# Performance work log

Measured on AMD Instinct MI355X. Metric: run time of the kernel, lower is better.

The kernel has to match this reference:

```python
import jax, jax.numpy as jnp
import numpy as np

NUM_QUBITS = 16
N_LAYERS = 3
N_PARAMS = 6
BATCH = 64
DIM = 2 ** NUM_QUBITS


def setup_inputs() -> dict:
    key = jax.random.key(0)
    k1, k2, k3, k4, k5 = jax.random.split(key, 5)
    sr = jax.random.normal(k1, (BATCH, DIM), jnp.float32)
    si = jax.random.normal(k2, (BATCH, DIM), jnp.float32)
    nrm = jnp.sqrt(jnp.sum(sr * sr + si * si, axis=1, keepdims=True))
    sr, si = sr / nrm, si / nrm  # StatePrep requires normalized states
    var_params = jax.random.normal(k3, (N_LAYERS, NUM_QUBITS, N_PARAMS), jnp.float32)
    head_w = jax.random.normal(k4, (1, NUM_QUBITS), jnp.float32) / np.sqrt(NUM_QUBITS)
    head_b = jax.random.normal(k5, (1,), jnp.float32) * 0.01
    return {"state_real": sr, "state_imag": si, "var_params": var_params,
            "head_w": head_w, "head_b": head_b}


def _rot_unitary(tx, ty, tz):
    # Fused single-qubit unitary U = RZ(tz) @ RY(ty) @ RX(tx)
    cx, sx = jnp.cos(tx / 2), jnp.sin(tx / 2)
    cy, sy = jnp.cos(ty / 2), jnp.sin(ty / 2)
    Rx = jnp.stack([jnp.stack([cx + 0j, -1j * sx]),
                    jnp.stack([-1j * sx, cx + 0j])])
    Ry = jnp.stack([jnp.stack([cy + 0j, -sy + 0j]),
                    jnp.stack([sy + 0j, cy + 0j])])
    ez = jnp.exp(-1j * tz / 2)
    zero = jnp.zeros_like(ez)
    Rz = jnp.stack([jnp.stack([ez, zero]), jnp.stack([zero, jnp.conj(ez)])])
    return (Rz @ Ry @ Rx).astype(jnp.complex64)


def _circuit_features(state_real, state_imag, var_params):
    psi = jax.lax.complex(state_real, state_imag)  # (B, 2^n), wire 0 = MSB
    B = psi.shape[0]
    for l in range(N_LAYERS):
        for q in range(NUM_QUBITS):
            U = _rot_unitary(var_params[l, q, 0], var_params[l, q, 1], var_params[l, q, 2])
            psi = psi.reshape(B, 2 ** q, 2, -1)  # isolate wire q
            psi = jnp.einsum('ij,bljr->blir', U, psi)
        for q in range(NUM_QUBITS - 1):
            # CNOT(control=q, target=q+1): flip target axis where control=1
            psi = psi.reshape(B, 2 ** q, 2, 2, -1)
            psi = jnp.concatenate([psi[:, :, 0:1], psi[:, :, 1:2, ::-1]], axis=2)
        psi = psi.reshape(B, -1)
    probs = psi.real ** 2 + psi.imag ** 2  # (B, 2^n)
    feats = []
    for q in range(NUM_QUBITS):
        p = probs.reshape(B, 2 ** q, 2, -1)
        feats.append(p[:, :, 0, :].sum(axis=(1, 2)) - p[:, :, 1, :].sum(axis=(1, 2)))
    return jnp.stack(feats, axis=1)  # (B, n) expvals of PauliZ


def reference(state_real, state_imag, var_params, head_w, head_b):
    feats = _circuit_features(state_real, state_imag, var_params)
    return (feats @ head_w.T + head_b)[:, 0]  # (B,)
```

## Files before the change

### kernel.cpp

```cpp
#include <hip/hip_runtime.h>


struct G8 { float r00,i00,r01,i01,r10,i10,r11,i11; };

__device__ __forceinline__ G8 loadG(const float* p) {
  G8 g;
  g.r00=p[0]; g.i00=p[1]; g.r01=p[2]; g.i01=p[3];
  g.r10=p[4]; g.i10=p[5]; g.r11=p[6]; g.i11=p[7];
  return g;
}

__device__ __forceinline__ void cmul2(const G8& g, float& r0, float& i0, float& r1, float& i1) {
  const float nr0 = g.r00*r0 - g.i00*i0 + g.r01*r1 - g.i01*i1;
  const float ni0 = g.r00*i0 + g.i00*r0 + g.r01*i1 + g.i01*r1;
  const float nr1 = g.r10*r0 - g.i10*i0 + g.r11*r1 - g.i11*i1;
  const float ni1 = g.r10*i0 + g.i10*r0 + g.r11*i1 + g.i11*r1;
  r0=nr0; i0=ni0; r1=nr1; i1=ni1;
}

__device__ __forceinline__ void cgate(const G8& g, int flip,
                                      float& r0, float& i0, float& r1, float& i1) {
  if (flip) cmul2(g, r1, i1, r0, i0);
  else      cmul2(g, r0, i0, r1, i1);
}

__device__ __forceinline__ void supd(const G8& g, int w, float& xr_, float& xi_,
                                     float pr, float pi_) {
  const float dr = w ? g.r11 : g.r00, di = w ? g.i11 : g.i00;
  const float br = w ? g.r10 : g.r01, bi = w ? g.i10 : g.i01;
  const float nr = dr*xr_ - di*xi_ + br*pr - bi*pi_;
  const float ni = dr*xi_ + di*xr_ + br*pi_ + bi*pr;
  xr_ = nr; xi_ = ni;
}

__device__ __forceinline__ void buildU(const float* __restrict__ vp, float* U) {
  const int i = threadIdx.x;
  if (i < 48) {
    const float tx = vp[i*6+0], ty = vp[i*6+1], tz = vp[i*6+2];
    float sx, cx, sy, cy, sz, cz;
    sincosf(0.5f*tx, &sx, &cx);
    sincosf(0.5f*ty, &sy, &cy);
    sincosf(0.5f*tz, &sz, &cz);
    const float m00r = cy*cx,  m00i = sy*sx;
    const float m01r = -sy*cx, m01i = -cy*sx;
    const float m10r = sy*cx,  m10i = -cy*sx;
    const float m11r = cy*cx,  m11i = -sy*sx;
    float* o = U + i*8;
    o[0] = cz*m00r + sz*m00i;  o[1] = cz*m00i - sz*m00r;
    o[2] = cz*m01r + sz*m01i;  o[3] = cz*m01i - sz*m01r;
    o[4] = cz*m10r - sz*m10i;  o[5] = cz*m10i + sz*m10r;
    o[6] = cz*m11r - sz*m11i;  o[7] = cz*m11i + sz*m11r;
  }
}

#define GU(l, w) loadG(Ush + ((l)*16 + (w))*8)

__global__ void __launch_bounds__(256, 2)
kA(const float* __restrict__ sr, const float* __restrict__ si,
   float* __restrict__ dr, float* __restrict__ di,
   const float* __restrict__ vp, const float* __restrict__ hb, float* __restrict__ out) {
  __shared__ float Ush[384];
  buildU(vp, Ush);
  const int t = threadIdx.x;
  const int l = t & 63, wv = t >> 6;
  const int l5 = (l >> 5) & 1, l4 = (l >> 4) & 1;
  const int b = blockIdx.x >> 3, c = blockIdx.x & 7;
  if (blockIdx.x == 0 && t < 64) out[t] = hb[0];
  __syncthreads();

  const size_t bb = (size_t)b << 16;
  const int tb = (l5 << 10) | (l4 << 9) | (c << 6) | (wv << 4) | (l & 15);
  float xr[32], xi[32];
  #pragma unroll
  for (int k = 0; k < 32; ++k) {
    xr[k] = sr[bb + (k << 11) + tb];
    xi[k] = si[bb + (k << 11) + tb];
  }

  #pragma unroll
  for (int g = 0; g < 5; ++g) {
    const int kb = 4 - g;
    const G8 U = GU(0, g);
    #pragma unroll
    for (int p = 0; p < 16; ++p) {
      const int i0 = ((p >> kb) << (kb + 1)) | (p & ((1 << kb) - 1));
      cmul2(U, xr[i0], xi[i0], xr[i0 | (1 << kb)], xi[i0 | (1 << kb)]);
    }
  }
  { const G8 U = GU(0, 5);
    #pragma unroll
    for (int a = 0; a < 32; ++a) {
      const float pr = __shfl_xor(xr[a], 32), pi_ = __shfl_xor(xi[a], 32);
      supd(U, l5, xr[a], xi[a], pr, pi_);
    } }
  { const G8 U = GU(0, 6);
    #pragma unroll
    for (int a = 0; a < 32; ++a) {
      const float pr = __shfl_xor(xr[a], 16), pi_ = __shfl_xor(xi[a], 16);
      supd(U, l4, xr[a], xi[a], pr, pi_);
    } }
  { const G8 U = GU(1, 0);
    #pragma unroll
    for (int k = 0; k < 32; ++k) if (!((k >> 4) & 1))
      cmul2(U, xr[k], xi[k], xr[k^24], xi[k^24]); }
  { const G8 U = GU(1, 1);
    #pragma unroll
    for (int k = 0; k < 32; ++k) if (!((k >> 3) & 1))
      cgate(U, (k >> 4) & 1, xr[k], xi[k], xr[k^12], xi[k^12]); }
  { const G8 U = GU(1, 2);
    #pragma unroll
    for (int k = 0; k < 32; ++k) if (!((k >> 2) & 1))
      cgate(U, ((k>>4)^(k>>3)) & 1, xr[k], xi[k], xr[k^6], xi[k^6]); }
  { const G8 U = GU(1, 3);
    #pragma unroll
    for (int k = 0; k < 32; ++k) if (!((k >> 1) & 1))
      cgate(U, ((k>>4)^(k>>3)^(k>>2)) & 1, xr[k], xi[k], xr[k^3], xi[k^3]); }
  { const G8 U = GU(1, 4);
    #pragma unroll
    for (int m = 0; m < 16; ++m) {
      const int k0 = 2*m, k1 = 2*m + 1;
      const float p0r = __shfl_xor(xr[k1], 32), p0i = __shfl_xor(xi[k1], 32);
      const float p1r = __shfl_xor(xr[k0], 32), p1i = __shfl_xor(xi[k0], 32);
      const int w0 = __builtin_popcount(k0) & 1;
      supd(U, w0,     xr[k0], xi[k0], p0r, p0i);
      supd(U, w0 ^ 1, xr[k1], xi[k1], p1r, p1i);
    } }
  { const G8 U = GU(1, 5);
    #pragma unroll
    for (int k = 0; k < 32; ++k) {
      const float pr = __shfl_xor(xr[k], 48), pi_ = __shfl_xor(xi[k], 48);
      supd(U, (__builtin_popcount(k) ^ l5) & 1, xr[k], xi[k], pr, pi_);
    } }
  { const G8 U = GU(2, 0);
    #pragma unroll
    for (int k = 0; k < 32; ++k) if (!((k >> 4) & 1))
      cmul2(U, xr[k], xi[k], xr[k^20], xi[k^20]); }
  { const G8 U = GU(2, 1);
    #pragma unroll
    for (int k = 0; k < 32; ++k) if (!((k >> 3) & 1))
      cmul2(U, xr[k], xi[k], xr[k^10], xi[k^10]); }
  { const G8 U = GU(2, 2);
    #pragma unroll
    for (int k = 0; k < 32; ++k) if (!((k >> 2) & 1))
      cgate(U, (k >> 4) & 1, xr[k], xi[k], xr[k^5], xi[k^5]); }
  { const G8 U = GU(2, 3);
    #pragma unroll
    for (int k = 0; k < 32; ++k) if (!((k >> 1) & 1)) {
      const float p0r = __shfl_xor(xr[k^2], 32), p0i = __shfl_xor(xi[k^2], 32);
      const float p1r = __shfl_xor(xr[k],   32), p1i = __shfl_xor(xi[k],   32);
      const int w0 = (k >> 3) & 1;
      supd(U, w0,     xr[k],   xi[k],   p0r, p0i);
      supd(U, w0 ^ 1, xr[k^2], xi[k^2], p1r, p1i);
    } }

  #pragma unroll
  for (int k = 0; k < 32; ++k) {
    dr[bb + (k << 11) + tb] = xr[k];
    di[bb + (k << 11) + tb] = xi[k];
  }
}

__device__ __forceinline__ int SA(int a) { return a ^ ((a >> 6) & 3); }

__global__ void __launch_bounds__(256, 2)
kB(const float* __restrict__ sr, const float* __restrict__ si,
   const float* __restrict__ vp, const float* __restrict__ hw, float* __restrict__ out) {
  __shared__ float lds[8192];
  __shared__ float Ush[384];
  __shared__ float red[4];
  buildU(vp, Ush);
  const int t = threadIdx.x;
  const int l = t & 63, wv = t >> 6;
  const int b = blockIdx.x >> 4, h = blockIdx.x & 15;
  __syncthreads();

  const int ph = __builtin_popcount(h) & 1;
  const int pA = ((h >> 1) ^ (h >> 3)) & 1;
  const int pB = (h ^ (h >> 2)) & 1;
  const size_t base0 = ((size_t)b << 16) | (h << 12) | (wv << 8) | (l << 2);

  float xr[16], xi[16];
  #pragma unroll
  for (int k = 0; k < 4; ++k) {
    const float4 vr = *(const float4*)(sr + base0 + (k << 10));
    const float4 vi = *(const float4*)(si + base0 + (k << 10));
    xr[k*4+0]=vr.x; xr[k*4+1]=vr.y; xr[k*4+2]=vr.z; xr[k*4+3]=vr.w;
    xi[k*4+0]=vi.x; xi[k*4+1]=vi.y; xi[k*4+2]=vi.z; xi[k*4+3]=vi.w;
  }

  #pragma unroll
  for (int g = 0; g < 6; ++g) {
    const int mask = 32 >> g;
    const G8 U = GU(0, 8 + g);
    const int hi = (l >> (5 - g)) & 1;
    #pragma unroll
    for (int a = 0; a < 16; ++a) {
      const float pr = __shfl_xor(xr[a], mask), pi_ = __shfl_xor(xi[a], mask);
      supd(U, hi, xr[a], xi[a], pr, pi_);
    }
  }
  { const G8 U = GU(0, 14);
    #pragma unroll
    for (int k = 0; k < 4; ++k) {
      cmul2(U, xr[k*4+0], xi[k*4+0], xr[k*4+2], xi[k*4+2]);
      cmul2(U, xr[k*4+1], xi[k*4+1], xr[k*4+3], xi[k*4+3]);
    } }
  { const G8 U = GU(0, 15);
    #pragma unroll
    for (int k = 0; k < 4; ++k) {
      cmul2(U, xr[k*4+0], xi[k*4+0], xr[k*4+1], xi[k*4+1]);
      cmul2(U, xr[k*4+2], xi[k*4+2], xr[k*4+3], xi[k*4+3]);
    } }

  #pragma unroll
  for (int k = 0; k < 4; ++k)
    #pragma unroll
    for (int e = 0; e < 4; ++e) {
      const int a = (k << 10) | (wv << 8) | (l << 2) | e;
      lds[SA(a)]        = xr[k*4+e];
      lds[4096 + SA(a)] = xi[k*4+e];
    }
  __syncthreads();
  float yr[16], yi[16];
  #pragma unroll
  for (int m = 0; m < 16; ++m) {
    const int a2 = (m << 8) | (l << 2) | wv;
    yr[m] = lds[SA(a2)];
    yi[m] = lds[4096 + SA(a2)];
  }

  const int l5 = (l>>5)&1, l4 = (l>>4)&1, l3 = (l>>3)&1, l2 = (l>>2)&1, l1 = (l>>1)&1;
  { const G8 U = GU(0, 7);
    #pragma unroll
    for (int m = 0; m < 16; ++m) if (!(m & 1))
      cmul2(U, yr[m], yi[m], yr[m^1], yi[m^1]); }
  { const G8 U = GU(1, 6);
    #pragma unroll
    for (int m = 0; m < 16; ++m) if (!((m >> 1) & 1))
      cgate(U, ((m>>2) ^ (m>>3) ^ ph) & 1, yr[m], yi[m], yr[m^3], yi[m^3]); }
  { const G8 U = GU(1, 7);
    #pragma unroll
    for (int m = 0; m < 16; m += 2) {
      const float p0r = __shfl_xor(yr[m+1], 32), p0i = __shfl_xor(yi[m+1], 32);
      const float p1r = __shfl_xor(yr[m],   32), p1i = __shfl_xor(yi[m],   32);
      const int w0 = (__builtin_popcount(m) ^ ph) & 1;
      supd(U, w0,     yr[m],   yi[m],   p0r, p0i);
      supd(U, w0 ^ 1, yr[m+1], yi[m+1], p1r, p1i);
    } }
  #pragma unroll
  for (int g = 0; g < 5; ++g) {
    const int mask = 48 >> g;
    const G8 U = GU(1, 8 + g);
    int lp;
    if      (g == 0) lp = l5;
    else if (g == 1) lp = l4 ^ l5;
    else if (g == 2) lp = l3 ^ l4 ^ l5;
    else if (g == 3) lp = l2 ^ l3 ^ l4 ^ l5;
    else             lp = l1 ^ l2 ^ l3 ^ l4 ^ l5;
    #pragma unroll
    for (int m = 0; m < 16; ++m) {
      const float pr = __shfl_xor(yr[m], mask), pi_ = __shfl_xor(yi[m], mask);
      supd(U, (lp ^ __builtin_popcount(m) ^ ph) & 1, yr[m], yi[m], pr, pi_);
    }
  }
  { const G8 U = GU(2, 4);
    #pragma unroll
    for (int m = 0; m < 16; ++m) if (!((m >> 3) & 1))
      cgate(U, pA, yr[m], yi[m], yr[m^10], yi[m^10]); }
  { const G8 U = GU(2, 5);
    #pragma unroll
    for (int m = 0; m < 16; ++m) if (!((m >> 2) & 1))
      cgate(U, pB, yr[m], yi[m], yr[m^5], yi[m^5]); }
  { const G8 U = GU(2, 6);
    #pragma unroll
    for (int m = 0; m < 16; ++m) if (!((m >> 1) & 1)) {
      const float p0r = __shfl_xor(yr[m^2], 32), p0i = __shfl_xor(yi[m^2], 32);
      const float p1r = __shfl_xor(yr[m],   32), p1i = __shfl_xor(yi[m],   32);
      const int w0 = ((m >> 3) ^ pA) & 1;
      supd(U, w0,     yr[m],   yi[m],   p0r, p0i);
      supd(U, w0 ^ 1, yr[m^2], yi[m^2], p1r, p1i);
    } }
  { const G8 U = GU(2, 7);
    #pragma unroll
    for (int m = 0; m < 16; m += 2) {
      const float p0r = __shfl_xor(yr[m+1], 16), p0i = __shfl_xor(yi[m+1], 16);
      const float p1r = __shfl_xor(yr[m],   16), p1i = __shfl_xor(yi[m],   16);
      const int w0 = ((m >> 2) ^ pB) & 1;
      supd(U, w0,     yr[m],   yi[m],   p0r, p0i);
      supd(U, w0 ^ 1, yr[m+1], yi[m+1], p1r, p1i);
    } }
  #pragma unroll
  for (int g = 0; g < 3; ++g) {
    const int mask = (g == 0) ? 40 : (g == 1) ? 20 : 10;
    const G8 U = GU(2, 8 + g);
    int lp, mpar, hp;
    if      (g == 0) { lp = l5;      mpar = 0x0A; hp = pA; }
    else if (g == 1) { lp = l4;      mpar = 0x05; hp = pB; }
    else             { lp = l3 ^ l5; mpar = 0x0A; hp = pA; }
    #pragma unroll
    for (int m = 0; m < 16; ++m) {
      const float pr = __shfl_xor(yr[m], mask), pi_ = __shfl_xor(yi[m], mask);
      supd(U, (lp ^ __builtin_popcount(m & mpar) ^ hp) & 1, yr[m], yi[m], pr, pi_);
    }
  }

  __syncthreads();
  #pragma unroll
  for (int m = 0; m < 16; ++m) {
    const int a2 = (m << 8) | (l << 2) | wv;
    lds[SA(a2)]        = yr[m];
    lds[4096 + SA(a2)] = yi[m];
  }
  __syncthreads();
  #pragma unroll
  for (int k = 0; k < 4; ++k)
    #pragma unroll
    for (int e = 0; e < 4; ++e) {
      const int a = (k << 10) | (wv << 8) | (l << 2) | e;
      xr[k*4+e] = lds[SA(a)];
      xi[k*4+e] = lds[4096 + SA(a)];
    }

  const int wv1 = (wv >> 1) & 1, wv0 = wv & 1;
  const int l0 = l & 1;
  const int RP   = (__builtin_popcount(l) ^ __builtin_popcount(wv) ^ ph) & 1;
  const int oddT = (l1 ^ l3 ^ l5 ^ wv1 ^ pA) & 1;
  const int evT  = (l0 ^ l2 ^ l4 ^ wv0 ^ pB) & 1;
  { const G8 U = GU(1, 13);
    #pragma unroll
    for (int k = 0; k < 4; ++k) {
      const int w = (RP ^ __builtin_popcount(k)) & 1;
      #pragma unroll
      for (int e0 = 0; e0 < 2; ++e0) {
        const int a = k*4 + e0, a2 = k*4 + e0 + 2;
        const float par = __shfl_xor(xr[a2], 1), pai = __shfl_xor(xi[a2], 1);
        const float pbr = __shfl_xor(xr[a],  1), pbi = __shfl_xor(xi[a],  1);
        supd(U, w, xr[a],  xi[a],  par, pai);
        supd(U, w, xr[a2], xi[a2], pbr, pbi);
      }
    } }
  { const G8 U = GU(1, 14);
    #pragma unroll
    for (int k = 0; k < 4; ++k) {
      const int f = (RP ^ __builtin_popcount(k)) & 1;
      cgate(U, f, xr[k*4+0], xi[k*4+0], xr[k*4+3], xi[k*4+3]);
      cgate(U, f, xr[k*4+1], xi[k*4+1], xr[k*4+2], xi[k*4+2]);
    } }
  { const G8 U = GU(1, 15);
    #pragma unroll
    for (int k = 0; k < 4; ++k) {
      const int f = (RP ^ __builtin_popcount(k)) & 1;
      cgate(U, f,     xr[k*4+0], xi[k*4+0], xr[k*4+1], xi[k*4+1]);
      cgate(U, f ^ 1, xr[k*4+2], xi[k*4+2], xr[k*4+3], xi[k*4+3]);
    } }
  { const G8 U = GU(2, 11);
    const int base4 = (l2 ^ l4 ^ wv0 ^ pB) & 1;
    #pragma unroll
    for (int a = 0; a < 16; ++a) {
      const float pr = __shfl_xor(xr[a], 5), pi_ = __shfl_xor(xi[a], 5);
      supd(U, (base4 ^ (a >> 2)) & 1, xr[a], xi[a], pr, pi_);
    } }
  { const G8 U = GU(2, 12);
    #pragma unroll
    for (int k = 0; k < 4; ++k) {
      const int w = (oddT ^ (k >> 1)) & 1;
      #pragma unroll
      for (int e0 = 0; e0 < 2; ++e0) {
        const int a = k*4 + e0, a2 = k*4 + e0 + 2;
        const float par = __shfl_xor(xr[a2], 2), pai = __shfl_xor(xi[a2], 2);
        const float pbr = __shfl_xor(xr[a],  2), pbi = __shfl_xor(xi[a],  2);
        supd(U, w, xr[a],  xi[a],  par, pai);
        supd(U, w, xr[a2], xi[a2], pbr, pbi);
      }
    } }
  { const G8 U = GU(2, 13);
    #pragma unroll
    for (int k = 0; k < 4; ++k) {
      const int w = (evT ^ k) & 1;
      #pragma unroll
      for (int e0 = 0; e0 < 4; e0 += 2) {
        const int a = k*4 + e0, a2 = k*4 + e0 + 1;
        const float par = __shfl_xor(xr[a2], 1), pai = __shfl_xor(xi[a2], 1);
        const float pbr = __shfl_xor(xr[a],  1), pbi = __shfl_xor(xi[a],  1);
        supd(U, w, xr[a],  xi[a],  par, pai);
        supd(U, w, xr[a2], xi[a2], pbr, pbi);
      }
    } }
  { const G8 U = GU(2, 14);
    #pragma unroll
    for (int k = 0; k < 4; ++k) {
      const int f = (oddT ^ (k >> 1)) & 1;
      cgate(U, f, xr[k*4+0], xi[k*4+0], xr[k*4+2], xi[k*4+2]);
      cgate(U, f, xr[k*4+1], xi[k*4+1], xr[k*4+3], xi[k*4+3]);
    } }
  { const G8 U = GU(2, 15);
    #pragma unroll
    for (int k = 0; k < 4; ++k) {
      const int f = (evT ^ k) & 1;
      cgate(U, f, xr[k*4+0], xi[k*4+0], xr[k*4+1], xi[k*4+1]);
      cgate(U, f, xr[k*4+2], xi[k*4+2], xr[k*4+3], xi[k*4+3]);
    } }

  float p_[16];
  #pragma unroll
  for (int a = 0; a < 16; ++a) p_[a] = xr[a]*xr[a] + xi[a]*xi[a];
  const int jloc = (h << 12) | (wv << 8) | (l << 2);
  float hsum = 0.f;
  #pragma unroll
  for (int q = 0; q < 16; ++q) {
    const int M = (0x3333 << (15 - q)) & 0xFFFF;
    float s = 0.f;
    #pragma unroll
    for (int k = 0; k < 4; ++k)
      #pragma unroll
      for (int e = 0; e < 4; ++e) {
        const int amp = (k << 10) | e;
        s += (__builtin_popcount(amp & M) & 1) ? -p_[k*4+e] : p_[k*4+e];
      }
    if (__builtin_popcount(jloc & M) & 1) s = -s;
    hsum += hw[q] * s;
  }
  #pragma unroll
  for (int o = 32; o >= 1; o >>= 1) hsum += __shfl_xor(hsum, o);
  __syncthreads();
  if ((t & 63) == 0) red[wv] = hsum;
  __syncthreads();
  if (t == 0) atomicAdd(out + b, red[0] + red[1] + red[2] + red[3]);
}

extern "C" void kernel_launch(void* const* d_in, const int* in_sizes, int n_in,
                              void* d_out, int out_size, void* d_ws, size_t ws_size,
                              hipStream_t stream) {
  const float* in_r = (const float*)d_in[0];
  const float* in_i = (const float*)d_in[1];
  const float* vp = (const float*)d_in[2];
  const float* hw = (const float*)d_in[3];
  const float* hb = (const float*)d_in[4];
  float* out = (float*)d_out;

  float* ws_r = (float*)d_ws;
  float* ws_i = ws_r + 4194304ull;

  kA<<<512,  256, 0, stream>>>(in_r, in_i, ws_r, ws_i, vp, hb, out);
  kB<<<1024, 256, 0, stream>>>(ws_r, ws_i, vp, hw, out);
}
```

Before: 148.5 us.

## Pack complex amplitudes into float2 vectors and fold an extra qubit into registers

Amplitudes are now held as two-wide float vectors so the complex gate math maps onto packed FMA instructions (v_pk_fma on CDNA). In kA each vector is a (real, imag) pair. In kB each vector pairs two amplitudes that differ in qubit 3, so each thread holds 32 amplitudes and the grid halves to 512 blocks with a doubled LDS transpose buffer. Gates on that qubit are moved from layer 1/2 into the in-register section with swizzled pairing, and the gate assignment across the two kB phases is reshuffled. This is meant to cut ALU instruction count and block count. In exchange it raises register and LDS pressure, which can lower occupancy, and it changes a lot of the parity bookkeeping.

```diff
diff --git a/kernel.cpp b/kernel.cpp
--- a/kernel.cpp
+++ b/kernel.cpp
@@ -1,7 +1,16 @@
 #include <hip/hip_runtime.h>
 
 
+typedef float f2 __attribute__((ext_vector_type(2)));
+
 struct G8 { float r00,i00,r01,i01,r10,i10,r11,i11; };
+
+__device__ __forceinline__ f2 mkf2(float a, float b) { f2 r; r.x = a; r.y = b; return r; }
+__device__ __forceinline__ f2 swp(f2 v) { f2 r; r.x = v.y; r.y = v.x; return r; }
+__device__ __forceinline__ f2 sn(f2 v) { f2 r; r.x = -v.y; r.y = v.x; return r; }
+__device__ __forceinline__ f2 shf2(f2 v, int mask) {
+  return mkf2(__shfl_xor(v.x, mask), __shfl_xor(v.y, mask));
+}
 
 __device__ __forceinline__ G8 loadG(const float* p) {
   G8 g;
@@ -10,27 +19,37 @@
   return g;
 }
 
-__device__ __forceinline__ void cmul2(const G8& g, float& r0, float& i0, float& r1, float& i1) {
-  const float nr0 = g.r00*r0 - g.i00*i0 + g.r01*r1 - g.i01*i1;
-  const float ni0 = g.r00*i0 + g.i00*r0 + g.r01*i1 + g.i01*r1;
-  const float nr1 = g.r10*r0 - g.i10*i0 + g.r11*r1 - g.i11*i1;
-  const float ni1 = g.r10*i0 + g.i10*r0 + g.r11*i1 + g.i11*r1;
-  r0=nr0; i0=ni0; r1=nr1; i1=ni1;
-}
-
-__device__ __forceinline__ void cgate(const G8& g, int flip,
-                                      float& r0, float& i0, float& r1, float& i1) {
-  if (flip) cmul2(g, r1, i1, r0, i0);
-  else      cmul2(g, r0, i0, r1, i1);
-}
-
-__device__ __forceinline__ void supd(const G8& g, int w, float& xr_, float& xi_,
-                                     float pr, float pi_) {
-  const float dr = w ? g.r11 : g.r00, di = w ? g.i11 : g.i00;
-  const float br = w ? g.r10 : g.r01, bi = w ? g.i10 : g.i01;
-  const float nr = dr*xr_ - di*xi_ + br*pr - bi*pi_;
-  const float ni = dr*xi_ + di*xr_ + br*pi_ + bi*pr;
-  xr_ = nr; xi_ = ni;
+struct CP { f2 dr, di, br, bi; };
+__device__ __forceinline__ CP mkCP(const G8& g, int w) {
+  CP c;
+  const float a = w ? g.r11 : g.r00, b = w ? g.i11 : g.i00;
+  const float p = w ? g.r10 : g.r01, q = w ? g.i10 : g.i01;
+  c.dr = mkf2(a,a); c.di = mkf2(b,b); c.br = mkf2(p,p); c.bi = mkf2(q,q);
+  return c;
+}
+__device__ __forceinline__ void supdP(const CP& c, f2& x, f2 p) {
+  x = __builtin_elementwise_fma(c.dr, x,
+       __builtin_elementwise_fma(c.di, sn(x),
+        __builtin_elementwise_fma(c.br, p, c.bi * sn(p))));
+}
+
+struct C2 { f2 dr, di, br, bi; };
+__device__ __forceinline__ C2 mkC2(const G8& g, int wlo, int whi) {
+  C2 c;
+  c.dr = mkf2(wlo ? g.r11 : g.r00, whi ? g.r11 : g.r00);
+  c.di = mkf2(wlo ? g.i11 : g.i00, whi ? g.i11 : g.i00);
+  c.br = mkf2(wlo ? g.r10 : g.r01, whi ? g.r10 : g.r01);
+  c.bi = mkf2(wlo ? g.i10 : g.i01, whi ? g.i10 : g.i01);
+  return c;
+}
+__device__ __forceinline__ void supd2(const C2& c, f2& xr, f2& xi, f2 pr, f2 pi) {
+  f2 nr = __builtin_elementwise_fma(c.dr, xr,
+           __builtin_elementwise_fma(c.di, -xi,
+            __builtin_elementwise_fma(c.br, pr, c.bi * (-pi))));
+  f2 ni = __builtin_elementwise_fma(c.dr, xi,
+           __builtin_elementwise_fma(c.di, xr,
+            __builtin_elementwise_fma(c.br, pi, c.bi * pr)));
+  xr = nr; xi = ni;
 }
 
 __device__ __forceinline__ void buildU(const float* __restrict__ vp, float* U) {
@@ -70,362 +89,379 @@
 
   const size_t bb = (size_t)b << 16;
   const int tb = (l5 << 10) | (l4 << 9) | (c << 6) | (wv << 4) | (l & 15);
-  float xr[32], xi[32];
+  f2 x[32];
   #pragma unroll
   for (int k = 0; k < 32; ++k) {
-    xr[k] = sr[bb + (k << 11) + tb];
-    xi[k] = si[bb + (k << 11) + tb];
-  }
+    const size_t a = bb + (k << 11) + tb;
+    x[k] = mkf2(sr[a], si[a]);
+  }
+
+#define RPA(CA, CB, A, B) { f2 tt = x[A]; supdP(CA, x[A], x[B]); supdP(CB, x[B], tt); }
 
   #pragma unroll
   for (int g = 0; g < 5; ++g) {
     const int kb = 4 - g;
     const G8 U = GU(0, g);
+    const CP c0 = mkCP(U, 0), c1 = mkCP(U, 1);
     #pragma unroll
     for (int p = 0; p < 16; ++p) {
       const int i0 = ((p >> kb) << (kb + 1)) | (p & ((1 << kb) - 1));
-      cmul2(U, xr[i0], xi[i0], xr[i0 | (1 << kb)], xi[i0 | (1 << kb)]);
+      RPA(c0, c1, i0, i0 | (1 << kb));
     }
   }
-  { const G8 U = GU(0, 5);
-    #pragma unroll
-    for (int a = 0; a < 32; ++a) {
-      const float pr = __shfl_xor(xr[a], 32), pi_ = __shfl_xor(xi[a], 32);
-      supd(U, l5, xr[a], xi[a], pr, pi_);
-    } }
-  { const G8 U = GU(0, 6);
-    #pragma unroll
-    for (int a = 0; a < 32; ++a) {
-      const float pr = __shfl_xor(xr[a], 16), pi_ = __shfl_xor(xi[a], 16);
-      supd(U, l4, xr[a], xi[a], pr, pi_);
-    } }
-  { const G8 U = GU(1, 0);
-    #pragma unroll
-    for (int k = 0; k < 32; ++k) if (!((k >> 4) & 1))
-      cmul2(U, xr[k], xi[k], xr[k^24], xi[k^24]); }
-  { const G8 U = GU(1, 1);
-    #pragma unroll
-    for (int k = 0; k < 32; ++k) if (!((k >> 3) & 1))
-      cgate(U, (k >> 4) & 1, xr[k], xi[k], xr[k^12], xi[k^12]); }
-  { const G8 U = GU(1, 2);
-    #pragma unroll
-    for (int k = 0; k < 32; ++k) if (!((k >> 2) & 1))
-      cgate(U, ((k>>4)^(k>>3)) & 1, xr[k], xi[k], xr[k^6], xi[k^6]); }
-  { const G8 U = GU(1, 3);
-    #pragma unroll
-    for (int k = 0; k < 32; ++k) if (!((k >> 1) & 1))
-      cgate(U, ((k>>4)^(k>>3)^(k>>2)) & 1, xr[k], xi[k], xr[k^3], xi[k^3]); }
-  { const G8 U = GU(1, 4);
+  { const G8 U = GU(0,5); const CP cc = mkCP(U, l5);
+    #pragma unroll
+    for (int a = 0; a < 32; ++a) supdP(cc, x[a], shf2(x[a], 32)); }
+  { const G8 U = GU(0,6); const CP cc = mkCP(U, l4);
+    #pragma unroll
+    for (int a = 0; a < 32; ++a) supdP(cc, x[a], shf2(x[a], 16)); }
+  { const G8 U = GU(1,0); const CP c0 = mkCP(U,0), c1 = mkCP(U,1);
+    #pragma unroll
+    for (int k = 0; k < 32; ++k) if (!((k>>4)&1)) RPA(c0, c1, k, k^24); }
+  { const G8 U = GU(1,1); const CP c0 = mkCP(U,0), c1 = mkCP(U,1);
+    #pragma unroll
+    for (int k = 0; k < 32; ++k) if (!((k>>3)&1)) {
+      const int f = (k>>4)&1;
+      RPA(f?c1:c0, f?c0:c1, k, k^12);
+    } }
+  { const G8 U = GU(1,2); const CP c0 = mkCP(U,0), c1 = mkCP(U,1);
+    #pragma unroll
+    for (int k = 0; k < 32; ++k) if (!((k>>2)&1)) {
+      const int f = ((k>>4)^(k>>3))&1;
+      RPA(f?c1:c0, f?c0:c1, k, k^6);
+    } }
+  { const G8 U = GU(1,3); const CP c0 = mkCP(U,0), c1 = mkCP(U,1);
+    #pragma unroll
+    for (int k = 0; k < 32; ++k) if (!((k>>1)&1)) {
+      const int f = ((k>>4)^(k>>3)^(k>>2))&1;
+      RPA(f?c1:c0, f?c0:c1, k, k^3);
+    } }
+  { const G8 U = GU(1,4); const CP c0 = mkCP(U,0), c1 = mkCP(U,1);
     #pragma unroll
     for (int m = 0; m < 16; ++m) {
-      const int k0 = 2*m, k1 = 2*m + 1;
-      const float p0r = __shfl_xor(xr[k1], 32), p0i = __shfl_xor(xi[k1], 32);
-      const float p1r = __shfl_xor(xr[k0], 32), p1i = __shfl_xor(xi[k0], 32);
-      const int w0 = __builtin_popcount(k0) & 1;
-      supd(U, w0,     xr[k0], xi[k0], p0r, p0i);
-      supd(U, w0 ^ 1, xr[k1], xi[k1], p1r, p1i);
-    } }
-  { const G8 U = GU(1, 5);
-    #pragma unroll
-    for (int k = 0; k < 32; ++k) {
-      const float pr = __shfl_xor(xr[k], 48), pi_ = __shfl_xor(xi[k], 48);
-      supd(U, (__builtin_popcount(k) ^ l5) & 1, xr[k], xi[k], pr, pi_);
-    } }
-  { const G8 U = GU(2, 0);
-    #pragma unroll
-    for (int k = 0; k < 32; ++k) if (!((k >> 4) & 1))
-      cmul2(U, xr[k], xi[k], xr[k^20], xi[k^20]); }
-  { const G8 U = GU(2, 1);
-    #pragma unroll
-    for (int k = 0; k < 32; ++k) if (!((k >> 3) & 1))
-      cmul2(U, xr[k], xi[k], xr[k^10], xi[k^10]); }
-  { const G8 U = GU(2, 2);
-    #pragma unroll
-    for (int k = 0; k < 32; ++k) if (!((k >> 2) & 1))
-      cgate(U, (k >> 4) & 1, xr[k], xi[k], xr[k^5], xi[k^5]); }
-  { const G8 U = GU(2, 3);
-    #pragma unroll
-    for (int k = 0; k < 32; ++k) if (!((k >> 1) & 1)) {
-      const float p0r = __shfl_xor(xr[k^2], 32), p0i = __shfl_xor(xi[k^2], 32);
-      const float p1r = __shfl_xor(xr[k],   32), p1i = __shfl_xor(xi[k],   32);
-      const int w0 = (k >> 3) & 1;
-      supd(U, w0,     xr[k],   xi[k],   p0r, p0i);
-      supd(U, w0 ^ 1, xr[k^2], xi[k^2], p1r, p1i);
+      const int k0 = 2*m, k1 = 2*m+1;
+      f2 p0 = shf2(x[k1], 32), p1 = shf2(x[k0], 32);
+      const int w0 = __builtin_popcount(k0)&1;
+      supdP(w0?c1:c0, x[k0], p0);
+      supdP(w0?c0:c1, x[k1], p1);
+    } }
+  { const G8 U = GU(2,0); const CP c0 = mkCP(U,0), c1 = mkCP(U,1);
+    #pragma unroll
+    for (int k = 0; k < 32; ++k) if (!((k>>4)&1)) RPA(c0, c1, k, k^20); }
+  { const G8 U = GU(2,1); const CP c0 = mkCP(U,0), c1 = mkCP(U,1);
+    #pragma unroll
+    for (int k = 0; k < 32; ++k) if (!((k>>3)&1)) RPA(c0, c1, k, k^10); }
+  { const G8 U = GU(2,2); const CP c0 = mkCP(U,0), c1 = mkCP(U,1);
+    #pragma unroll
+    for (int k = 0; k < 32; ++k) if (!((k>>2)&1)) {
+      const int f = (k>>4)&1;
+      RPA(f?c1:c0, f?c0:c1, k, k^5);
     } }
 
   #pragma unroll
   for (int k = 0; k < 32; ++k) {
-    dr[bb + (k << 11) + tb] = xr[k];
-    di[bb + (k << 11) + tb] = xi[k];
-  }
-}
-
-__device__ __forceinline__ int SA(int a) { return a ^ ((a >> 6) & 3); }
+    const size_t a = bb + (k << 11) + tb;
+    dr[a] = x[k].x; di[a] = x[k].y;
+  }
+#undef RPA
+}
+
+__device__ __forceinline__ int SA2(int i) { return i ^ (((i >> 5) & 7) << 1); }
 
 __global__ void __launch_bounds__(256, 2)
 kB(const float* __restrict__ sr, const float* __restrict__ si,
    const float* __restrict__ vp, const float* __restrict__ hw, float* __restrict__ out) {
-  __shared__ float lds[8192];
+  __shared__ float lds[16384];
   __shared__ float Ush[384];
   __shared__ float red[4];
   buildU(vp, Ush);
   const int t = threadIdx.x;
   const int l = t & 63, wv = t >> 6;
-  const int b = blockIdx.x >> 4, h = blockIdx.x & 15;
-  __syncthreads();
-
-  const int ph = __builtin_popcount(h) & 1;
-  const int pA = ((h >> 1) ^ (h >> 3)) & 1;
-  const int pB = (h ^ (h >> 2)) & 1;
-  const size_t base0 = ((size_t)b << 16) | (h << 12) | (wv << 8) | (l << 2);
-
-  float xr[16], xi[16];
-  #pragma unroll
-  for (int k = 0; k < 4; ++k) {
-    const float4 vr = *(const float4*)(sr + base0 + (k << 10));
-    const float4 vi = *(const float4*)(si + base0 + (k << 10));
-    xr[k*4+0]=vr.x; xr[k*4+1]=vr.y; xr[k*4+2]=vr.z; xr[k*4+3]=vr.w;
-    xi[k*4+0]=vi.x; xi[k*4+1]=vi.y; xi[k*4+2]=vi.z; xi[k*4+3]=vi.w;
-  }
+  const int b = blockIdx.x >> 3, h3 = blockIdx.x & 7;
+  __syncthreads();
+
+  const int P   = __builtin_popcount(h3) & 1;
+  const int h14 = (h3 >> 1) & 1;
+  const int pA  = (h3 ^ (h3 >> 2)) & 1;
+  const size_t base0 = ((size_t)b << 16) | (h3 << 13) | (wv << 8) | (l << 2);
+
+  f2 xr2[16], xi2[16];
+  #pragma unroll
+  for (int kk = 0; kk < 4; ++kk) {
+    const float4 r0 = *(const float4*)(sr + base0 + (kk << 10));
+    const float4 r1 = *(const float4*)(sr + base0 + (kk << 10) + 4096);
+    const float4 i0 = *(const float4*)(si + base0 + (kk << 10));
+    const float4 i1 = *(const float4*)(si + base0 + (kk << 10) + 4096);
+    xr2[kk*4+0] = mkf2(r0.x, r1.x); xr2[kk*4+1] = mkf2(r0.y, r1.y);
+    xr2[kk*4+2] = mkf2(r0.z, r1.z); xr2[kk*4+3] = mkf2(r0.w, r1.w);
+    xi2[kk*4+0] = mkf2(i0.x, i1.x); xi2[kk*4+1] = mkf2(i0.y, i1.y);
+    xi2[kk*4+2] = mkf2(i0.z, i1.z); xi2[kk*4+3] = mkf2(i0.w, i1.w);
+  }
+
+#define RP2(CA, CB, A, B) { f2 tr = xr2[A], ti = xi2[A]; \
+    supd2(CA, xr2[A], xi2[A], xr2[B], xi2[B]); \
+    supd2(CB, xr2[B], xi2[B], tr, ti); }
 
   #pragma unroll
   for (int g = 0; g < 6; ++g) {
     const int mask = 32 >> g;
     const G8 U = GU(0, 8 + g);
     const int hi = (l >> (5 - g)) & 1;
-    #pragma unroll
-    for (int a = 0; a < 16; ++a) {
-      const float pr = __shfl_xor(xr[a], mask), pi_ = __shfl_xor(xi[a], mask);
-      supd(U, hi, xr[a], xi[a], pr, pi_);
+    const C2 cc = mkC2(U, hi, hi);
+    #pragma unroll
+    for (int s = 0; s < 16; ++s) {
+      f2 pr = shf2(xr2[s], mask), pi = shf2(xi2[s], mask);
+      supd2(cc, xr2[s], xi2[s], pr, pi);
     }
   }
-  { const G8 U = GU(0, 14);
-    #pragma unroll
-    for (int k = 0; k < 4; ++k) {
-      cmul2(U, xr[k*4+0], xi[k*4+0], xr[k*4+2], xi[k*4+2]);
-      cmul2(U, xr[k*4+1], xi[k*4+1], xr[k*4+3], xi[k*4+3]);
-    } }
-  { const G8 U = GU(0, 15);
-    #pragma unroll
-    for (int k = 0; k < 4; ++k) {
-      cmul2(U, xr[k*4+0], xi[k*4+0], xr[k*4+1], xi[k*4+1]);
-      cmul2(U, xr[k*4+2], xi[k*4+2], xr[k*4+3], xi[k*4+3]);
-    } }
-
-  #pragma unroll
-  for (int k = 0; k < 4; ++k)
-    #pragma unroll
-    for (int e = 0; e < 4; ++e) {
-      const int a = (k << 10) | (wv << 8) | (l << 2) | e;
-      lds[SA(a)]        = xr[k*4+e];
-      lds[4096 + SA(a)] = xi[k*4+e];
-    }
-  __syncthreads();
-  float yr[16], yi[16];
+  { const G8 U = GU(0,14);
+    const C2 c0 = mkC2(U,0,0), c1 = mkC2(U,1,1);
+    #pragma unroll
+    for (int kk = 0; kk < 4; ++kk)
+      #pragma unroll
+      for (int e0 = 0; e0 < 2; ++e0) RP2(c0, c1, kk*4+e0, kk*4+e0+2); }
+  { const G8 U = GU(0,15);
+    const C2 c0 = mkC2(U,0,0), c1 = mkC2(U,1,1);
+    #pragma unroll
+    for (int kk = 0; kk < 4; ++kk) {
+      RP2(c0, c1, kk*4+0, kk*4+1);
+      RP2(c0, c1, kk*4+2, kk*4+3);
+    } }
+
+  #pragma unroll
+  for (int s = 0; s < 16; ++s) {
+    const int i0 = (((s >> 2) << 10) | (wv << 8) | (l << 2) | (s & 3)) << 1;
+    *(f2*)&lds[SA2(i0)] = xr2[s];
+    *(f2*)&lds[8192 + SA2(i0)] = xi2[s];
+  }
+  __syncthreads();
   #pragma unroll
   for (int m = 0; m < 16; ++m) {
-    const int a2 = (m << 8) | (l << 2) | wv;
-    yr[m] = lds[SA(a2)];
-    yi[m] = lds[4096 + SA(a2)];
-  }
-
-  const int l5 = (l>>5)&1, l4 = (l>>4)&1, l3 = (l>>3)&1, l2 = (l>>2)&1, l1 = (l>>1)&1;
-  { const G8 U = GU(0, 7);
-    #pragma unroll
-    for (int m = 0; m < 16; ++m) if (!(m & 1))
-      cmul2(U, yr[m], yi[m], yr[m^1], yi[m^1]); }
-  { const G8 U = GU(1, 6);
-    #pragma unroll
-    for (int m = 0; m < 16; ++m) if (!((m >> 1) & 1))
-      cgate(U, ((m>>2) ^ (m>>3) ^ ph) & 1, yr[m], yi[m], yr[m^3], yi[m^3]); }
-  { const G8 U = GU(1, 7);
+    const int i2 = (((m << 8) | (l << 2) | wv)) << 1;
+    xr2[m] = *(f2*)&lds[SA2(i2)];
+    xi2[m] = *(f2*)&lds[8192 + SA2(i2)];
+  }
+
+  const int l5=(l>>5)&1, l4=(l>>4)&1, l3=(l>>3)&1, l2=(l>>2)&1, l1=(l>>1)&1, l0=l&1;
+  { const G8 U = GU(0,7);
+    const C2 c0 = mkC2(U,0,0), c1 = mkC2(U,1,1);
+    #pragma unroll
+    for (int m = 0; m < 16; m += 2) RP2(c0, c1, m, m^1); }
+  { const G8 U = GU(1,5);
+    const C2 cA = mkC2(U, P, P^1), cB = mkC2(U, P^1, P);
+    #pragma unroll
+    for (int m = 0; m < 16; ++m) if (!((m>>2)&1)) {
+      const int f = (m>>3)&1;
+      RP2(f?cB:cA, f?cA:cB, m, m^6);
+    } }
+  { const G8 U = GU(1,6);
+    const C2 cA = mkC2(U, P, P^1), cB = mkC2(U, P^1, P);
+    #pragma unroll
+    for (int m = 0; m < 16; ++m) if (!((m>>1)&1)) {
+      const int f = ((m>>3)^(m>>2))&1;
+      RP2(f?cB:cA, f?cA:cB, m, m^3);
+    } }
+  { const G8 U = GU(1,7);
+    const C2 cA = mkC2(U, P, P^1), cB = mkC2(U, P^1, P);
     #pragma unroll
     for (int m = 0; m < 16; m += 2) {
-      const float p0r = __shfl_xor(yr[m+1], 32), p0i = __shfl_xor(yi[m+1], 32);
-      const float p1r = __shfl_xor(yr[m],   32), p1i = __shfl_xor(yi[m],   32);
-      const int w0 = (__builtin_popcount(m) ^ ph) & 1;
-      supd(U, w0,     yr[m],   yi[m],   p0r, p0i);
-      supd(U, w0 ^ 1, yr[m+1], yi[m+1], p1r, p1i);
+      f2 p0r = shf2(xr2[m^1],32), p0i = shf2(xi2[m^1],32);
+      f2 p1r = shf2(xr2[m],32),   p1i = shf2(xi2[m],32);
+      const int f = __builtin_popcount(m)&1;
+      supd2(f?cB:cA, xr2[m], xi2[m], p0r, p0i);
+      supd2(f?cA:cB, xr2[m^1], xi2[m^1], p1r, p1i);
     } }
   #pragma unroll
   for (int g = 0; g < 5; ++g) {
     const int mask = 48 >> g;
     const G8 U = GU(1, 8 + g);
-    int lp;
-    if      (g == 0) lp = l5;
-    else if (g == 1) lp = l4 ^ l5;
-    else if (g == 2) lp = l3 ^ l4 ^ l5;
-    else if (g == 3) lp = l2 ^ l3 ^ l4 ^ l5;
-    else             lp = l1 ^ l2 ^ l3 ^ l4 ^ l5;
+    const int lp = (g==0)? l5 : (g==1)? (l4^l5) : (g==2)? (l3^l4^l5)
+                 : (g==3)? (l2^l3^l4^l5) : (l1^l2^l3^l4^l5);
+    const C2 cA = mkC2(U, lp^P, lp^P^1), cB = mkC2(U, lp^P^1, lp^P);
     #pragma unroll
     for (int m = 0; m < 16; ++m) {
-      const float pr = __shfl_xor(yr[m], mask), pi_ = __shfl_xor(yi[m], mask);
-      supd(U, (lp ^ __builtin_popcount(m) ^ ph) & 1, yr[m], yi[m], pr, pi_);
+      f2 pr = shf2(xr2[m], mask), pi = shf2(xi2[m], mask);
+      supd2((__builtin_popcount(m)&1)?cB:cA, xr2[m], xi2[m], pr, pi);
     }
   }
-  { const G8 U = GU(2, 4);
-    #pragma unroll
-    for (int m = 0; m < 16; ++m) if (!((m >> 3) & 1))
-      cgate(U, pA, yr[m], yi[m], yr[m^10], yi[m^10]); }
-  { const G8 U = GU(2, 5);
-    #pragma unroll
-    for (int m = 0; m < 16; ++m) if (!((m >> 2) & 1))
-      cgate(U, pB, yr[m], yi[m], yr[m^5], yi[m^5]); }
-  { const G8 U = GU(2, 6);
-    #pragma unroll
-    for (int m = 0; m < 16; ++m) if (!((m >> 1) & 1)) {
-      const float p0r = __shfl_xor(yr[m^2], 32), p0i = __shfl_xor(yi[m^2], 32);
-      const float p1r = __shfl_xor(yr[m],   32), p1i = __shfl_xor(yi[m],   32);
-      const int w0 = ((m >> 3) ^ pA) & 1;
-      supd(U, w0,     yr[m],   yi[m],   p0r, p0i);
-      supd(U, w0 ^ 1, yr[m^2], yi[m^2], p1r, p1i);
-    } }
-  { const G8 U = GU(2, 7);
+  { const G8 U = GU(2,3);
+    const C2 cc = mkC2(U, h14, h14^1);
+    #pragma unroll
+    for (int m = 0; m < 16; ++m) if (!((m>>2)&1)) {
+      f2 tr = xr2[m], ti = xi2[m];
+      supd2(cc, xr2[m], xi2[m], swp(xr2[m^4]), swp(xi2[m^4]));
+      supd2(cc, xr2[m^4], xi2[m^4], swp(tr), swp(ti));
+    } }
+  { const G8 U = GU(2,4);
+    const C2 cA = mkC2(U, pA, pA), cB = mkC2(U, pA^1, pA^1);
+    #pragma unroll
+    for (int m = 0; m < 16; ++m) if (!((m>>3)&1)) RP2(cA, cB, m, m^10); }
+  { const G8 U = GU(2,5);
+    const C2 cA = mkC2(U, h14, h14^1), cB = mkC2(U, h14^1, h14);
+    #pragma unroll
+    for (int m = 0; m < 16; ++m) if (!((m>>2)&1)) RP2(cA, cB, m, m^5); }
+  { const G8 U = GU(2,6);
+    const C2 cA = mkC2(U, pA, pA), cB = mkC2(U, pA^1, pA^1);
+    #pragma unroll
+    for (int m = 0; m < 16; ++m) if (!((m>>1)&1)) {
+      f2 p0r = shf2(xr2[m^2],32), p0i = shf2(xi2[m^2],32);
+      f2 p1r = shf2(xr2[m],32),   p1i = shf2(xi2[m],32);
+      const int f = (m>>3)&1;
+      supd2(f?cB:cA, xr2[m], xi2[m], p0r, p0i);
+      supd2(f?cA:cB, xr2[m^2], xi2[m^2], p1r, p1i);
+    } }
+  { const G8 U = GU(2,7);
+    const C2 cA = mkC2(U, h14, h14^1), cB = mkC2(U, h14^1, h14);
     #pragma unroll
     for (int m = 0; m < 16; m += 2) {
-      const float p0r = __shfl_xor(yr[m+1], 16), p0i = __shfl_xor(yi[m+1], 16);
-      const float p1r = __shfl_xor(yr[m],   16), p1i = __shfl_xor(yi[m],   16);
-      const int w0 = ((m >> 2) ^ pB) & 1;
-      supd(U, w0,     yr[m],   yi[m],   p0r, p0i);
-      supd(U, w0 ^ 1, yr[m+1], yi[m+1], p1r, p1i);
+      f2 p0r = shf2(xr2[m^1],16), p0i = shf2(xi2[m^1],16);
+      f2 p1r = shf2(xr2[m],16),   p1i = shf2(xi2[m],16);
+      const int f = (m>>2)&1;
+      supd2(f?cB:cA, xr2[m], xi2[m], p0r, p0i);
+      supd2(f?cA:cB, xr2[m^1], xi2[m^1], p1r, p1i);
     } }
   #pragma unroll
   for (int g = 0; g < 3; ++g) {
     const int mask = (g == 0) ? 40 : (g == 1) ? 20 : 10;
     const G8 U = GU(2, 8 + g);
-    int lp, mpar, hp;
-    if      (g == 0) { lp = l5;      mpar = 0x0A; hp = pA; }
-    else if (g == 1) { lp = l4;      mpar = 0x05; hp = pB; }
-    else             { lp = l3 ^ l5; mpar = 0x0A; hp = pA; }
+    int lp, mpar, blo, bhi;
+    if      (g == 0) { lp = l5;      mpar = 0x0A; blo = lp^pA;  bhi = lp^pA; }
+    else if (g == 1) { lp = l4;      mpar = 0x05; blo = lp^h14; bhi = lp^h14^1; }
+    else             { lp = l3^l5;   mpar = 0x0A; blo = lp^pA;  bhi = lp^pA; }
+    const C2 cA = mkC2(U, blo, bhi), cB = mkC2(U, blo^1, bhi^1);
     #pragma unroll
     for (int m = 0; m < 16; ++m) {
-      const float pr = __shfl_xor(yr[m], mask), pi_ = __shfl_xor(yi[m], mask);
-      supd(U, (lp ^ __builtin_popcount(m & mpar) ^ hp) & 1, yr[m], yi[m], pr, pi_);
+      f2 pr = shf2(xr2[m], mask), pi = shf2(xi2[m], mask);
+      supd2((__builtin_popcount(m & mpar)&1)?cB:cA, xr2[m], xi2[m], pr, pi);
     }
   }
 
   __syncthreads();
   #pragma unroll
   for (int m = 0; m < 16; ++m) {
-    const int a2 = (m << 8) | (l << 2) | wv;
-    lds[SA(a2)]        = yr[m];
-    lds[4096 + SA(a2)] = yi[m];
-  }
-  __syncthreads();
-  #pragma unroll
-  for (int k = 0; k < 4; ++k)
-    #pragma unroll
-    for (int e = 0; e < 4; ++e) {
-      const int a = (k << 10) | (wv << 8) | (l << 2) | e;
-      xr[k*4+e] = lds[SA(a)];
-      xi[k*4+e] = lds[4096 + SA(a)];
-    }
+    const int i2 = (((m << 8) | (l << 2) | wv)) << 1;
+    *(f2*)&lds[SA2(i2)] = xr2[m];
+    *(f2*)&lds[8192 + SA2(i2)] = xi2[m];
+  }
+  __syncthreads();
+  #pragma unroll
+  for (int s = 0; s < 16; ++s) {
+    const int i0 = (((s >> 2) << 10) | (wv << 8) | (l << 2) | (s & 3)) << 1;
+    xr2[s] = *(f2*)&lds[SA2(i0)];
+    xi2[s] = *(f2*)&lds[8192 + SA2(i0)];
+  }
 
   const int wv1 = (wv >> 1) & 1, wv0 = wv & 1;
-  const int l0 = l & 1;
-  const int RP   = (__builtin_popcount(l) ^ __builtin_popcount(wv) ^ ph) & 1;
+  const int RPlo = (__builtin_popcount(l) ^ __builtin_popcount(wv) ^ P) & 1;
   const int oddT = (l1 ^ l3 ^ l5 ^ wv1 ^ pA) & 1;
-  const int evT  = (l0 ^ l2 ^ l4 ^ wv0 ^ pB) & 1;
-  { const G8 U = GU(1, 13);
-    #pragma unroll
-    for (int k = 0; k < 4; ++k) {
-      const int w = (RP ^ __builtin_popcount(k)) & 1;
+  const int evlo = (l0 ^ l2 ^ l4 ^ wv0 ^ h14) & 1;
+  { const G8 U = GU(1,13);
+    const C2 cA = mkC2(U, RPlo, RPlo^1), cB = mkC2(U, RPlo^1, RPlo);
+    #pragma unroll
+    for (int kk = 0; kk < 4; ++kk) {
+      const C2& cc = (__builtin_popcount(kk)&1) ? cB : cA;
       #pragma unroll
       for (int e0 = 0; e0 < 2; ++e0) {
-        const int a = k*4 + e0, a2 = k*4 + e0 + 2;
-        const float par = __shfl_xor(xr[a2], 1), pai = __shfl_xor(xi[a2], 1);
-        const float pbr = __shfl_xor(xr[a],  1), pbi = __shfl_xor(xi[a],  1);
-        supd(U, w, xr[a],  xi[a],  par, pai);
-        supd(U, w, xr[a2], xi[a2], pbr, pbi);
+        const int a = kk*4 + e0, a2 = a + 2;
+        f2 par = shf2(xr2[a2],1), pai = shf2(xi2[a2],1);
+        f2 pbr = shf2(xr2[a],1),  pbi = shf2(xi2[a],1);
+        supd2(cc, xr2[a],  xi2[a],  par, pai);
+        supd2(cc, xr2[a2], xi2[a2], pbr, pbi);
       }
     } }
-  { const G8 U = GU(1, 14);
-    #pragma unroll
-    for (int k = 0; k < 4; ++k) {
-      const int f = (RP ^ __builtin_popcount(k)) & 1;
-      cgate(U, f, xr[k*4+0], xi[k*4+0], xr[k*4+3], xi[k*4+3]);
-      cgate(U, f, xr[k*4+1], xi[k*4+1], xr[k*4+2], xi[k*4+2]);
-    } }
-  { const G8 U = GU(1, 15);
-    #pragma unroll
-    for (int k = 0; k < 4; ++k) {
-      const int f = (RP ^ __builtin_popcount(k)) & 1;
-      cgate(U, f,     xr[k*4+0], xi[k*4+0], xr[k*4+1], xi[k*4+1]);
-      cgate(U, f ^ 1, xr[k*4+2], xi[k*4+2], xr[k*4+3], xi[k*4+3]);
-    } }
-  { const G8 U = GU(2, 11);
-    const int base4 = (l2 ^ l4 ^ wv0 ^ pB) & 1;
-    #pragma unroll
-    for (int a = 0; a < 16; ++a) {
-      const float pr = __shfl_xor(xr[a], 5), pi_ = __shfl_xor(xi[a], 5);
-      supd(U, (base4 ^ (a >> 2)) & 1, xr[a], xi[a], pr, pi_);
-    } }
-  { const G8 U = GU(2, 12);
-    #pragma unroll
-    for (int k = 0; k < 4; ++k) {
-      const int w = (oddT ^ (k >> 1)) & 1;
+  { const G8 U = GU(1,14);
+    const C2 cA = mkC2(U, RPlo, RPlo^1), cB = mkC2(U, RPlo^1, RPlo);
+    #pragma unroll
+    for (int kk = 0; kk < 4; ++kk) {
+      const int f = __builtin_popcount(kk)&1;
+      RP2(f?cB:cA, f?cA:cB, kk*4+0, kk*4+3);
+      RP2(f?cB:cA, f?cA:cB, kk*4+1, kk*4+2);
+    } }
+  { const G8 U = GU(1,15);
+    const C2 cA = mkC2(U, RPlo, RPlo^1), cB = mkC2(U, RPlo^1, RPlo);
+    #pragma unroll
+    for (int kk = 0; kk < 4; ++kk) {
+      const int f = __builtin_popcount(kk)&1;
+      RP2(f?cB:cA, f?cA:cB, kk*4+0, kk*4+1);
+      RP2(f?cA:cB, f?cB:cA, kk*4+2, kk*4+3);
+    } }
+  { const G8 U = GU(2,11);
+    const int b4 = (l2 ^ l4 ^ wv0) & 1;
+    const C2 cA = mkC2(U, b4^h14, b4^h14^1), cB = mkC2(U, b4^h14^1, b4^h14);
+    #pragma unroll
+    for (int s = 0; s < 16; ++s) {
+      f2 pr = shf2(xr2[s], 5), pi = shf2(xi2[s], 5);
+      supd2(((s>>2)&1)?cB:cA, xr2[s], xi2[s], pr, pi);
+    } }
+  { const G8 U = GU(2,12);
+    const C2 cA = mkC2(U, oddT, oddT), cB = mkC2(U, oddT^1, oddT^1);
+    #pragma unroll
+    for (int kk = 0; kk < 4; ++kk) {
+      const C2& cc = ((kk>>1)&1) ? cB : cA;
       #pragma unroll
       for (int e0 = 0; e0 < 2; ++e0) {
-        const int a = k*4 + e0, a2 = k*4 + e0 + 2;
-        const float par = __shfl_xor(xr[a2], 2), pai = __shfl_xor(xi[a2], 2);
-        const float pbr = __shfl_xor(xr[a],  2), pbi = __shfl_xor(xi[a],  2);
-        supd(U, w, xr[a],  xi[a],  par, pai);
-        supd(U, w, xr[a2], xi[a2], pbr, pbi);
+        const int a = kk*4 + e0, a2 = a + 2;
+        f2 par = shf2(xr2[a2],2), pai = shf2(xi2[a2],2);
+        f2 pbr = shf2(xr2[a],2),  pbi = shf2(xi2[a],2);
+        supd2(cc, xr2[a],  xi2[a],  par, pai);
+        supd2(cc, xr2[a2], xi2[a2], pbr, pbi);
       }
     } }
-  { const G8 U = GU(2, 13);
-    #pragma unroll
-    for (int k = 0; k < 4; ++k) {
-      const int w = (evT ^ k) & 1;
+  { const G8 U = GU(2,13);
+    const C2 cA = mkC2(U, evlo, evlo^1), cB = mkC2(U, evlo^1, evlo);
+    #pragma unroll
+    for (int kk = 0; kk < 4; ++kk) {
+      const C2& cc = (kk&1) ? cB : cA;
       #pragma unroll
       for (int e0 = 0; e0 < 4; e0 += 2) {
-        const int a = k*4 + e0, a2 = k*4 + e0 + 1;
-        const float par = __shfl_xor(xr[a2], 1), pai = __shfl_xor(xi[a2], 1);
-        const float pbr = __shfl_xor(xr[a],  1), pbi = __shfl_xor(xi[a],  1);
-        supd(U, w, xr[a],  xi[a],  par, pai);
-        supd(U, w, xr[a2], xi[a2], pbr, pbi);
+        const int a = kk*4 + e0, a2 = a + 1;
+        f2 par = shf2(xr2[a2],1), pai = shf2(xi2[a2],1);
+        f2 pbr = shf2(xr2[a],1),  pbi = shf2(xi2[a],1);
+        supd2(cc, xr2[a],  xi2[a],  par, pai);
+        supd2(cc, xr2[a2], xi2[a2], pbr, pbi);
       }
     } }
-  { const G8 U = GU(2, 14);
-    #pragma unroll
-    for (int k = 0; k < 4; ++k) {
-      const int f = (oddT ^ (k >> 1)) & 1;
-      cgate(U, f, xr[k*4+0], xi[k*4+0], xr[k*4+2], xi[k*4+2]);
-      cgate(U, f, xr[k*4+1], xi[k*4+1], xr[k*4+3], xi[k*4+3]);
-    } }
-  { const G8 U = GU(2, 15);
-    #pragma unroll
-    for (int k = 0; k < 4; ++k) {
-      const int f = (evT ^ k) & 1;
-      cgate(U, f, xr[k*4+0], xi[k*4+0], xr[k*4+1], xi[k*4+1]);
-      cgate(U, f, xr[k*4+2], xi[k*4+2], xr[k*4+3], xi[k*4+3]);
-    } }
-
-  float p_[16];
-  #pragma unroll
-  for (int a = 0; a < 16; ++a) p_[a] = xr[a]*xr[a] + xi[a]*xi[a];
-  const int jloc = (h << 12) | (wv << 8) | (l << 2);
+  { const G8 U = GU(2,14);
+    const C2 cA = mkC2(U, oddT, oddT), cB = mkC2(U, oddT^1, oddT^1);
+    #pragma unroll
+    for (int kk = 0; kk < 4; ++kk) {
+      const int f = (kk>>1)&1;
+      RP2(f?cB:cA, f?cA:cB, kk*4+0, kk*4+2);
+      RP2(f?cB:cA, f?cA:cB, kk*4+1, kk*4+3);
+    } }
+  { const G8 U = GU(2,15);
+    const C2 cA = mkC2(U, evlo, evlo^1), cB = mkC2(U, evlo^1, evlo);
+    #pragma unroll
+    for (int kk = 0; kk < 4; ++kk) {
+      const int f = kk&1;
+      RP2(f?cB:cA, f?cA:cB, kk*4+0, kk*4+1);
+      RP2(f?cB:cA, f?cA:cB, kk*4+2, kk*4+3);
+    } }
+
+  #pragma unroll
+  for (int s = 0; s < 16; ++s)
+    xr2[s] = xr2[s]*xr2[s] + xi2[s]*xi2[s];
+  const int jloc = (h3 << 13) | (wv << 8) | (l << 2);
   float hsum = 0.f;
   #pragma unroll
   for (int q = 0; q < 16; ++q) {
     const int M = (0x3333 << (15 - q)) & 0xFFFF;
-    float s = 0.f;
-    #pragma unroll
-    for (int k = 0; k < 4; ++k)
-      #pragma unroll
-      for (int e = 0; e < 4; ++e) {
-        const int amp = (k << 10) | e;
-        s += (__builtin_popcount(amp & M) & 1) ? -p_[k*4+e] : p_[k*4+e];
-      }
-    if (__builtin_popcount(jloc & M) & 1) s = -s;
-    hsum += hw[q] * s;
+    f2 acc = mkf2(0.f, 0.f);
+    #pragma unroll
+    for (int s = 0; s < 16; ++s) {
+      const int amp = ((s >> 2) << 10) | (s & 3);
+      if (__builtin_popcount(amp & M) & 1) acc -= xr2[s]; else acc += xr2[s];
+    }
+    float sv = acc.x + (((M >> 12) & 1) ? -acc.y : acc.y);
+    if (__builtin_popcount(jloc & M) & 1) sv = -sv;
+    hsum += hw[q] * sv;
   }
   #pragma unroll
   for (int o = 32; o >= 1; o >>= 1) hsum += __shfl_xor(hsum, o);
-  __syncthreads();
   if ((t & 63) == 0) red[wv] = hsum;
   __syncthreads();
   if (t == 0) atomicAdd(out + b, red[0] + red[1] + red[2] + red[3]);
+#undef RP2
 }
 
 extern "C" void kernel_launch(void* const* d_in, const int* in_sizes, int n_in,
@@ -441,6 +477,6 @@
   float* ws_r = (float*)d_ws;
   float* ws_i = ws_r + 4194304ull;
 
-  kA<<<512,  256, 0, stream>>>(in_r, in_i, ws_r, ws_i, vp, hb, out);
-  kB<<<1024, 256, 0, stream>>>(ws_r, ws_i, vp, hw, out);
-}
+  kA<<<512, 256, 0, stream>>>(in_r, in_i, ws_r, ws_i, vp, hb, out);
+  kB<<<512, 256, 0, stream>>>(ws_r, ws_i, vp, hw, out);
+}
```

Result: faster. 141.5 us (-4.8%).
